# Optimization experiments

Measured on AMD Instinct MI355X. Metric: run time of the kernel, lower is better.

Reference implementation:

```python
import jax, jax.numpy as jnp
import numpy as np
from jax import lax

V, E, H, B, T = 50000, 512, 512, 128, 256
OUT = 2

def gru(x, Wi, Wh, bi, bh):
    # x: [B,T,D]; PyTorch GRU equations, h0 = 0. Returns all hidden states [B,T,H].
    Bsz = x.shape[0]
    Hd = Wh.shape[1]
    xW = jnp.einsum('btd,gd->btg', x, Wi) + bi  # [B,T,3H], precompute input projections
    def step(h, xw):
        gh = h @ Wh.T + bh
        xr, xz, xn = jnp.split(xw, 3, axis=-1)
        hr, hz, hn = jnp.split(gh, 3, axis=-1)
        r = jax.nn.sigmoid(xr + hr)
        z = jax.nn.sigmoid(xz + hz)
        n = jnp.tanh(xn + r * hn)
        h_new = (1.0 - z) * n + z * h
        return h_new, h_new
    h0 = jnp.zeros((Bsz, Hd), x.dtype)
    _, hs = lax.scan(step, h0, jnp.swapaxes(xW, 0, 1))
    return jnp.swapaxes(hs, 0, 1)

def dual_attention(u, r, u_all_sum, Aw, bw, Ww):
    # u, r: [B,T,D] (query side / response side per timestep, vectorized over T).
    # w_t[b,t] = (u A^T + b) . r  (the original bmm of [B,1,D] x [B,D,1])
    w = jnp.einsum('btd,btd->bt', jnp.einsum('btd,ed->bte', u, Aw) + bw, r)
    # score = softmax over D of tanh(w) * Ww  (Linear(1, D, bias=False))
    sc = jax.nn.softmax(jnp.tanh(w)[..., None] * Ww[None, None, :], axis=-1)  # [B,T,D]
    # sum_s embed[b,s,:] * score[b,t,:] = score * (sum over time) ; then * r_t
    return sc * u_all_sum[:, None, :] * r  # [B,T,D]

def setup_inputs() -> dict:
    key = jax.random.key(0)
    ks = jax.random.split(key, 24)
    d = {}
    d['ask'] = jax.random.randint(ks[0], (B, T), 0, V, dtype=jnp.int32)
    d['answer'] = jax.random.randint(ks[1], (B, T), 0, V, dtype=jnp.int32)
    d['ask_keyword'] = jax.random.randint(ks[2], (B, T), 0, V, dtype=jnp.int32)
    d['answer_keyword'] = jax.random.randint(ks[3], (B, T), 0, V, dtype=jnp.int32)
    d['embed'] = jax.random.normal(ks[4], (V, E), jnp.float32) * 0.02
    # GRU 1: input E -> hidden H
    d['Wi1'] = jax.random.normal(ks[5], (3 * H, E), jnp.float32) * 0.05
    d['Wh1'] = jax.random.normal(ks[6], (3 * H, H), jnp.float32) * 0.05
    d['bi1'] = jnp.zeros((3 * H,), jnp.float32)
    d['bh1'] = jnp.zeros((3 * H,), jnp.float32)
    # word attention: Linear(E,E) + Linear(1,E,bias=False)
    d['Aw'] = jax.random.normal(ks[7], (E, E), jnp.float32) * 0.05
    d['bw'] = jnp.zeros((E,), jnp.float32)
    d['Ww'] = jax.random.normal(ks[8], (E,), jnp.float32) * 0.05
    # seq attention: Linear(H,H) + Linear(1,H,bias=False)
    d['As'] = jax.random.normal(ks[9], (H, H), jnp.float32) * 0.05
    d['bs'] = jnp.zeros((H,), jnp.float32)
    d['Ws'] = jax.random.normal(ks[10], (H,), jnp.float32) * 0.05
    # GRU 2: input E+H -> hidden H
    d['Wi2'] = jax.random.normal(ks[11], (3 * H, E + H), jnp.float32) * 0.05
    d['Wh2'] = jax.random.normal(ks[12], (3 * H, H), jnp.float32) * 0.05
    d['bi2'] = jnp.zeros((3 * H,), jnp.float32)
    d['bh2'] = jnp.zeros((3 * H,), jnp.float32)
    # final classifier
    d['Wf'] = jax.random.normal(ks[13], (OUT, H), jnp.float32) * 0.05
    d['bf'] = jnp.zeros((OUT,), jnp.float32)
    return d

def reference(ask, answer, ask_keyword, answer_keyword, embed, Wi1, Wh1, bi1, bh1,
              Aw, bw, Ww, As, bs, Ws, Wi2, Wh2, bi2, bh2, Wf, bf):
    ask_e = embed[ask]            # [B,T,E]
    ans_e = embed[answer]
    ask_kw = embed[ask_keyword]
    ans_kw = embed[answer_keyword]
    h_ask = gru(ask_e, Wi1, Wh1, bi1, bh1)  # [B,T,H]
    h_ans = gru(ans_e, Wi1, Wh1, bi1, bh1)
    # dual attention, vectorized over the original Python loop over t
    ctx_word = dual_attention(ask_kw, ans_kw, ask_kw.sum(axis=1), Aw, bw, Ww)   # [B,T,E]
    ctx_seq = dual_attention(h_ask, h_ans, h_ask.sum(axis=1), As, bs, Ws)       # [B,T,H]
    v = jnp.concatenate([ctx_word, ctx_seq], axis=-1)  # [B,T,E+H]
    h2 = gru(v, Wi2, Wh2, bi2, bh2)[:, -1, :]  # final hidden state [B,H]
    # dropout is identity in eval mode
    return jax.nn.softmax(h2 @ Wf.T + bf, axis=1)
```

## Files before the change

kernel.cpp:

```cpp
#include <hip/hip_runtime.h>
#include <cstdio>

typedef __bf16 bf16x8 __attribute__((ext_vector_type(8)));
typedef float f32x4 __attribute__((ext_vector_type(4)));

#define DEV __device__ __forceinline__

DEV short f2bf(float f) {
    unsigned u = __builtin_bit_cast(unsigned, f);
    u += 0x7fffu + ((u >> 16) & 1u);
    return (short)(u >> 16);
}
DEV float bf2f(short s) {
    unsigned u = ((unsigned)(unsigned short)s) << 16;
    return __builtin_bit_cast(float, u);
}
DEV float sigmoidf_(float x) { return 1.0f / (1.0f + __expf(-x)); }
DEV float tanhf_(float x) { float e = __expf(2.0f * x); return 1.0f - 2.0f / (e + 1.0f); }

DEV void gload_lds16(const void* g, void* l) {
    __builtin_amdgcn_global_load_lds(
        (__attribute__((address_space(1))) void*)(g),
        (__attribute__((address_space(3))) void*)(l), 16, 0, 0);
}
DEV f32x4 mfma16(bf16x8 a, bf16x8 b, f32x4 c) {
    return __builtin_amdgcn_mfma_f32_16x16x32_bf16(a, b, c, 0, 0, 0);
}
DEV unsigned ald(const unsigned* p) {
    return __hip_atomic_load(p, __ATOMIC_RELAXED, __HIP_MEMORY_SCOPE_AGENT);
}
DEV unsigned long long ald64(const void* p) {
    return __hip_atomic_load((const unsigned long long*)p, __ATOMIC_RELAXED, __HIP_MEMORY_SCOPE_AGENT);
}
DEV void ast64(void* p, unsigned long long v) {
    __hip_atomic_store((unsigned long long*)p, v, __ATOMIC_RELAXED, __HIP_MEMORY_SCOPE_AGENT);
}
DEV void ast32(void* p, unsigned v) {
    __hip_atomic_store((unsigned*)p, v, __ATOMIC_RELAXED, __HIP_MEMORY_SCOPE_AGENT);
}
DEV void aadd(unsigned* p, unsigned v) {
    __hip_atomic_fetch_add(p, v, __ATOMIC_RELAXED, __HIP_MEMORY_SCOPE_AGENT);
}

__global__ void f2bf_vec(const float* __restrict__ in, short* __restrict__ out, int n4) {
    int i = blockIdx.x * 256 + threadIdx.x;
    if (i >= n4) return;
    float4 v = reinterpret_cast<const float4*>(in)[i];
    short4 o;
    o.x = f2bf(v.x); o.y = f2bf(v.y); o.z = f2bf(v.z); o.w = f2bf(v.w);
    reinterpret_cast<short4*>(out)[i] = o;
}

__global__ void pack_wh(const float* __restrict__ Wh, short* __restrict__ Wp) {
    int tile = blockIdx.x, kk = blockIdx.y, l = threadIdx.x;
    int n = tile * 16 + (l & 15);
    int k0 = kk * 32 + (l >> 4) * 8;
    const float* src = Wh + (size_t)n * 512 + k0;
    short o[8];
#pragma unroll
    for (int e = 0; e < 8; e++) o[e] = f2bf(src[e]);
    *(int4*)(Wp + ((size_t)(tile * 16 + kk) * 64 + l) * 8) = *(int4*)o;
}

enum { A_XW1 = 0, A_UAW = 1, A_UAS = 2, A_XW2 = 3 };

template<int MODE>
DEV void gemm_tile(short* Als, short* Bls, short* Ct, int m0, int n0,
                   const short* Abase, const short* A2,
                   const int* tok0, const int* tok1,
                   const short* W, const float* bias, short* C, int N, int K)
{
    int tid = threadIdx.x;
    int l = tid & 63, w = tid >> 6;
    int wm = (w >> 1) * 64, wn = (w & 1) * 64;
    int kc = (tid & 7) * 8;

    const short* arow[4];
#pragma unroll
    for (int i = 0; i < 4; i++) {
        int gm = m0 + i * 32 + (tid >> 3);
        if (MODE == A_XW1) {
            int t = gm >> 8, s = gm & 255;
            int tok = (s < 128) ? tok0[s * 256 + t] : tok1[(s - 128) * 256 + t];
            arow[i] = Abase + (size_t)tok * 512;
        } else if (MODE == A_UAW) {
            int t = gm >> 7, b = gm & 127;
            arow[i] = Abase + (size_t)tok0[b * 256 + t] * 512;
        } else if (MODE == A_UAS) {
            int t = gm >> 7, b = gm & 127;
            arow[i] = Abase + ((size_t)t * 256 + b) * 512;
        } else {
            arow[i] = Abase + (size_t)gm * 512;
        }
    }

    f32x4 acc[4][4] = {};
    for (int kt = 0; kt < K; kt += 64) {
#pragma unroll
        for (int i = 0; i < 4; i++) {
            const short* asrc;
            if (MODE == A_XW2) {
                int gm = m0 + i * 32 + (tid >> 3);
                const short* base = (kt < 512) ? Abase : A2;
                asrc = base + (size_t)gm * 512 + (kt & 511) + kc;
            } else {
                asrc = arow[i] + kt + kc;
            }
            gload_lds16(asrc, Als + i * 2048 + tid * 8);
        }
#pragma unroll
        for (int i = 0; i < 4; i++)
            gload_lds16(W + (size_t)(n0 + i * 32 + (tid >> 3)) * K + kt + kc,
                        Bls + i * 2048 + tid * 8);
        __syncthreads();
#pragma unroll
        for (int kk = 0; kk < 2; kk++) {
            int ko = kk * 32 + (l >> 4) * 8;
            bf16x8 af[4], bfr[4];
#pragma unroll
            for (int mi = 0; mi < 4; mi++)
                af[mi] = *(const bf16x8*)&Als[(wm + mi * 16 + (l & 15)) * 64 + ko];
#pragma unroll
            for (int ni = 0; ni < 4; ni++)
                bfr[ni] = *(const bf16x8*)&Bls[(wn + ni * 16 + (l & 15)) * 64 + ko];
#pragma unroll
            for (int mi = 0; mi < 4; mi++)
#pragma unroll
                for (int ni = 0; ni < 4; ni++)
                    acc[mi][ni] = mfma16(af[mi], bfr[ni], acc[mi][ni]);
        }
        __syncthreads();
    }
#pragma unroll
    for (int ni = 0; ni < 4; ni++) {
        float bv = bias[n0 + wn + ni * 16 + (l & 15)];
#pragma unroll
        for (int mi = 0; mi < 4; mi++)
#pragma unroll
            for (int jj = 0; jj < 4; jj++)
                Ct[(wm + mi * 16 + (l >> 4) * 4 + jj) * 132 + wn + ni * 16 + (l & 15)] =
                    f2bf(acc[mi][ni][jj] + bv);
    }
    __syncthreads();
    for (int r = 0; r < 16; r++) {
        int idx = r * 256 + tid;
        int row = idx >> 5, cc = idx & 31;
        unsigned long long val = *(const unsigned long long*)(Ct + row * 132 + cc * 4);
        ast64(C + (size_t)(m0 + row) * N + n0 + cc * 4, val);
    }
    __syncthreads();
}

DEV void embed_sum_dev(const short* ebf, const int* tok, float* out, int b) {
    int d = threadIdx.x;
    float a0 = 0.f, a1 = 0.f;
    for (int t = 0; t < 256; t++) {
        const short* row = ebf + (size_t)tok[b * 256 + t] * 512;
        a0 += bf2f(row[d]); a1 += bf2f(row[d + 256]);
    }
    ast32(&out[b * 512 + d], __builtin_bit_cast(unsigned, a0));
    ast32(&out[b * 512 + d + 256], __builtin_bit_cast(unsigned, a1));
}
DEV void hall_sum_dev(const short* h_all, float* out, int b) {
    int d = threadIdx.x;
    float a0 = 0.f, a1 = 0.f;
    for (int t = 0; t < 256; t++) {
        const short* row = h_all + ((size_t)t * 256 + b) * 512;
        a0 += bf2f(row[d]); a1 += bf2f(row[d + 256]);
    }
    ast32(&out[b * 512 + d], __builtin_bit_cast(unsigned, a0));
    ast32(&out[b * 512 + d + 256], __builtin_bit_cast(unsigned, a1));
}

template<int WORD, int COHOUT>
DEV void combine4(int bb, const short* uA, const short* rsrc, const int* rtok,
                  const float* usum, const float* Wv, short* ctx)
{
    int l = threadIdx.x & 63, w = threadIdx.x >> 6;
    int m = bb * 4 + w;
    int t = m >> 7, b = m & 127;
    const short* rrow;
    if (WORD) rrow = rsrc + (size_t)rtok[b * 256 + t] * 512;
    else      rrow = rsrc + ((size_t)t * 256 + 128 + b) * 512;
    int d0 = l * 8;
    short ru[8], uu[8];
    *(int4*)ru = *(const int4*)(rrow + d0);
    *(unsigned long long*)uu       = ald64(uA + (size_t)m * 512 + d0);
    *((unsigned long long*)uu + 1) = ald64(uA + (size_t)m * 512 + d0 + 4);
    float rv[8], dot = 0.f;
#pragma unroll
    for (int i = 0; i < 8; i++) { rv[i] = bf2f(ru[i]); dot += rv[i] * bf2f(uu[i]); }
#pragma unroll
    for (int off = 32; off >= 1; off >>= 1) dot += __shfl_xor(dot, off);
    float tw = tanhf_(dot);
    float us[8];
#pragma unroll
    for (int i = 0; i < 4; i++) {
        unsigned long long uv = ald64(usum + b * 512 + d0 + i * 2);
        us[i * 2]     = __builtin_bit_cast(float, (unsigned)(uv & 0xffffffffu));
        us[i * 2 + 1] = __builtin_bit_cast(float, (unsigned)(uv >> 32));
    }
    float e[8], se = 0.f;
#pragma unroll
    for (int i = 0; i < 8; i++) { e[i] = __expf(tw * Wv[d0 + i]); se += e[i]; }
#pragma unroll
    for (int off = 32; off >= 1; off >>= 1) se += __shfl_xor(se, off);
    float inv = 1.f / se;
    short ov[8];
#pragma unroll
    for (int i = 0; i < 8; i++) ov[i] = f2bf(e[i] * inv * us[i] * rv[i]);
    if (COHOUT) {
        ast64(ctx + (size_t)m * 512 + d0,     *(unsigned long long*)ov);
        ast64(ctx + (size_t)m * 512 + d0 + 4, *((unsigned long long*)ov + 1));
    } else {
        *(int4*)(ctx + (size_t)m * 512 + d0) = *(int4*)ov;
    }
}

template<int WRITE_ALL>
DEV void scan_role(char* smem, int cb, int rg,
                   const short* xW, const short* Wp, const float* bh,
                   short* hb0, short* hb1, short* h_all, float* h_final,
                   unsigned* done, unsigned* slice_cnt, int tps, int S, int T)
{
    char* wl = smem;
    char* sl = smem + 98304;
    char* ho = smem + 131072;
    int tid = threadIdx.x;
    int r0 = rg * 32;
    int w = tid >> 6, l = tid & 63;
    int rt = w >> 1, ct = w & 1;
    int lrow = l & 15, lq = l >> 4;
    int colg = cb * 32 + ct * 16 + lrow;
    unsigned* mydone = done + rg * 32;

    for (int rr = 0; rr < 24; rr++) {
        int flat = rr * 256 + tid;
        int lane = flat & 63, kk = (flat >> 6) & 15, lg = flat >> 10;
        int g = lg >> 1, c2 = lg & 1;
        gload_lds16(Wp + (((size_t)(g * 32 + cb * 2 + c2) * 16 + kk) * 64 + lane) * 8,
                    wl + flat * 16);
    }
    float bhv[3];
#pragma unroll
    for (int g = 0; g < 3; g++) bhv[g] = bh[g * 512 + colg];
    __syncthreads();

    float hp[4] = {};

    for (int t = 0; t < T; t++) {
        if (tid < 16) {
            if (t > 0)
                while (ald(&mydone[tid]) < (unsigned)t) __builtin_amdgcn_s_sleep(1);
        } else if (tid == 16) {
            while (ald(&slice_cnt[t]) < (unsigned)tps) __builtin_amdgcn_s_sleep(1);
        }
        __syncthreads();

        short xrv[4], xzv[4], xnv[4];
        const short* xbase = xW + ((size_t)t * S + r0) * 1536 + colg;
#pragma unroll
        for (int j = 0; j < 4; j++) {
            const short* xp = xbase + (size_t)(rt * 16 + lq * 4 + j) * 1536;
            xrv[j] = xp[0]; xzv[j] = xp[512]; xnv[j] = xp[1024];
        }

        f32x4 acc[3] = {};
        if (t > 0) {
            const short* hprev = ((t & 1) ? hb0 : hb1) + (size_t)r0 * 512;
            unsigned long long v[16];
            const unsigned long long* sp = (const unsigned long long*)hprev;
#pragma unroll
            for (int k = 0; k < 16; k++)
                v[k] = ald64(sp + k * 256 + tid);
#pragma unroll
            for (int k = 0; k < 16; k++) {
                int off = (k * 256 + tid) * 8;
                int row = off >> 10, colb = off & 1023;
                *(unsigned long long*)(sl + row * 1024 + (colb ^ ((row & 7) << 4))) = v[k];
            }
            __syncthreads();
            bf16x8 afr[16];
            int ar = rt * 16 + lrow;
#pragma unroll
            for (int kk = 0; kk < 16; kk++) {
                int colb = kk * 64 + lq * 16;
                afr[kk] = *(const bf16x8*)(sl + ar * 1024 + (colb ^ ((ar & 7) << 4)));
            }
#pragma unroll
            for (int g = 0; g < 3; g++) {
                const char* bbase = wl + (size_t)((g * 2 + ct) * 16) * 1024 + l * 16;
#pragma unroll
                for (int kk = 0; kk < 16; kk++) {
                    bf16x8 bfr = *(const bf16x8*)(bbase + kk * 1024);
                    acc[g] = mfma16(afr[kk], bfr, acc[g]);
                }
            }
        }

        float hv[4];
#pragma unroll
        for (int j = 0; j < 4; j++) {
            float r = sigmoidf_(bf2f(xrv[j]) + bhv[0] + acc[0][j]);
            float z = sigmoidf_(bf2f(xzv[j]) + bhv[1] + acc[1][j]);
            float n = tanhf_(bf2f(xnv[j]) + r * (acc[2][j] + bhv[2]));
            hv[j] = (1.f - z) * n + z * hp[j];
            hp[j] = hv[j];
            *(short*)(ho + (rt * 16 + lq * 4 + j) * 72 + (ct * 16 + lrow) * 2) = f2bf(hv[j]);
        }
        __syncthreads();
        {
            int row = tid >> 3, ch = tid & 7;
            unsigned long long val = *(const unsigned long long*)(ho + row * 72 + ch * 8);
            short* hnew = (t & 1) ? hb1 : hb0;
            ast64(hnew + (size_t)(r0 + row) * 512 + cb * 32 + ch * 4, val);
            if (WRITE_ALL)
                *(unsigned long long*)(h_all + ((size_t)t * S + r0 + row) * 512 + cb * 32 + ch * 4) = val;
        }
        if (!WRITE_ALL && t == T - 1) {
#pragma unroll
            for (int j = 0; j < 4; j++)
                h_final[(size_t)(r0 + rt * 16 + lq * 4 + j) * 512 + colg] = hv[j];
        }
        __syncthreads();
        if (tid == 0)
            ast32(&mydone[cb], (unsigned)(t + 1));
    }
}

__global__ __launch_bounds__(256, 1) void gru_fused1(
    short* xW1, const short* __restrict__ Wp, const float* __restrict__ bh,
    short* __restrict__ hb0, short* __restrict__ hb1, short* __restrict__ h_all,
    unsigned* done, unsigned* slc,
    const short* __restrict__ embed_bf, const int* __restrict__ ask,
    const int* __restrict__ answer, const short* __restrict__ Wi1b,
    const float* __restrict__ bi1,
    const int* __restrict__ askkw, const int* __restrict__ anskw,
    const short* __restrict__ Awb, const float* __restrict__ bw,
    float* usumW, short* uAb, const float* __restrict__ Ww, short* ctxW,
    unsigned* wcnt)
{
    __shared__ char smem[133376];
    int bid = blockIdx.x, tid = threadIdx.x;

    if (bid >= 128) {
        int pid = bid - 128;
        short* Als = (short*)smem;
        short* Bls = (short*)(smem + 16384);
        short* Ct  = (short*)(smem + 32768);
        for (int q = pid; q < 256 * 24; q += 128) {
            int slice = q / 24, j = q % 24;
            int m0 = (slice * 2 + (j >= 12 ? 1 : 0)) * 128, n0 = (j % 12) * 128;
            gemm_tile<A_XW1>(Als, Bls, Ct, m0, n0, embed_bf, nullptr, ask, answer,
                             Wi1b, bi1, xW1, 1536, 512);
            if (tid == 0) aadd(&slc[slice], 1u);
        }
        embed_sum_dev(embed_bf, askkw, usumW, pid);
        for (int k = 0; k < 8; k++) {
            int q = pid + k * 128;
            gemm_tile<A_UAW>(Als, Bls, Ct, (q >> 2) * 128, (q & 3) * 128,
                             embed_bf, nullptr, askkw, nullptr, Awb, bw, uAb, 512, 512);
        }
        if (tid == 0) {
            aadd(wcnt, 1u);
            while (ald(wcnt) < 128u) __builtin_amdgcn_s_sleep(1);
        }
        __syncthreads();
        for (int bb = pid * 64; bb < pid * 64 + 64; bb++)
            combine4<1, 0>(bb, uAb, embed_bf, anskw, usumW, Ww, ctxW);
        return;
    }
    scan_role<1>(smem, bid & 15, bid >> 4, xW1, Wp, bh, hb0, hb1, h_all, nullptr,
                 done, slc, 24, 256, 256);
}

__global__ __launch_bounds__(256, 1) void gru_fused2(
    short* xW2, const short* __restrict__ Wp, const float* __restrict__ bh,
    short* __restrict__ hb0, short* __restrict__ hb1, float* __restrict__ h_final,
    unsigned* done, unsigned* slc,
    const short* __restrict__ h_all, float* usumS, short* uAb,
    const short* __restrict__ Asb, const float* __restrict__ bs,
    const float* __restrict__ Ws, short* ctxS, const short* __restrict__ ctxW,
    const short* __restrict__ Wi2b, const float* __restrict__ bi2,
    unsigned* acnt, unsigned* ccnt)
{
    __shared__ char smem[133376];
    int bid = blockIdx.x, tid = threadIdx.x;
    short* Als = (short*)smem;
    short* Bls = (short*)(smem + 16384);
    short* Ct  = (short*)(smem + 32768);

    if (bid < 128) hall_sum_dev(h_all, usumS, bid);
    for (int k = 0; k < 4; k++) {
        int q = bid + k * 256;
        gemm_tile<A_UAS>(Als, Bls, Ct, (q >> 2) * 128, (q & 3) * 128,
                         h_all, nullptr, nullptr, nullptr, Asb, bs, uAb, 512, 512);
    }
    if (tid == 0) {
        aadd(acnt, 1u);
        while (ald(acnt) < 256u) __builtin_amdgcn_s_sleep(1);
    }
    __syncthreads();
    for (int bb = bid * 32; bb < bid * 32 + 32; bb++)
        combine4<0, 1>(bb, uAb, h_all, nullptr, usumS, Ws, ctxS);
    __syncthreads();
    if (tid == 0) aadd(ccnt, 1u);

    if (bid >= 64) {
        int pid = bid - 64;
        if (tid == 0) { while (ald(ccnt) < 256u) __builtin_amdgcn_s_sleep(1); }
        __syncthreads();
        for (int q = pid; q < 256 * 12; q += 192) {
            int slice = q / 12, j = q % 12;
            gemm_tile<A_XW2>(Als, Bls, Ct, slice * 128, j * 128,
                             ctxW, ctxS, nullptr, nullptr, Wi2b, bi2, xW2, 1536, 1024);
            if (tid == 0) aadd(&slc[slice], 1u);
        }
        return;
    }
    scan_role<0>(smem, bid & 15, bid >> 4, xW2, Wp, bh, hb0, hb1, nullptr, h_final,
                 done, slc, 12, 128, 256);
}

__global__ void final_head_k(const float* __restrict__ h2, const float* __restrict__ Wf,
                             const float* __restrict__ bfv, float* __restrict__ out) {
    int b = blockIdx.x, l = threadIdx.x;
    float d0 = 0.f, d1 = 0.f;
    for (int k = l; k < 512; k += 64) {
        float h = h2[b * 512 + k];
        d0 += h * Wf[k];
        d1 += h * Wf[512 + k];
    }
#pragma unroll
    for (int off = 32; off >= 1; off >>= 1) { d0 += __shfl_xor(d0, off); d1 += __shfl_xor(d1, off); }
    if (l == 0) {
        float l0 = d0 + bfv[0], l1 = d1 + bfv[1];
        float mx = fmaxf(l0, l1);
        float e0 = __expf(l0 - mx), e1 = __expf(l1 - mx);
        float s = e0 + e1;
        out[b * 2] = e0 / s; out[b * 2 + 1] = e1 / s;
    }
}

extern "C" void kernel_launch(void* const* d_in, const int* in_sizes, int n_in,
                              void* d_out, int out_size, void* d_ws, size_t ws_size,
                              hipStream_t stream)
{
    const int* ask    = (const int*)d_in[0];
    const int* answer = (const int*)d_in[1];
    const int* askkw  = (const int*)d_in[2];
    const int* anskw  = (const int*)d_in[3];
    const float* embed = (const float*)d_in[4];
    const float* Wi1 = (const float*)d_in[5];
    const float* Wh1 = (const float*)d_in[6];
    const float* bi1 = (const float*)d_in[7];
    const float* bh1 = (const float*)d_in[8];
    const float* Aw  = (const float*)d_in[9];
    const float* bw  = (const float*)d_in[10];
    const float* Ww  = (const float*)d_in[11];
    const float* As  = (const float*)d_in[12];
    const float* bs  = (const float*)d_in[13];
    const float* Ws  = (const float*)d_in[14];
    const float* Wi2 = (const float*)d_in[15];
    const float* Wh2 = (const float*)d_in[16];
    const float* bi2 = (const float*)d_in[17];
    const float* bh2 = (const float*)d_in[18];
    const float* Wf  = (const float*)d_in[19];
    const float* bfv = (const float*)d_in[20];

    char* ws = (char*)d_ws;
    size_t off = 0;
    auto alloc = [&](size_t bytes) -> void* {
        void* p = (void*)(ws + off);
        off += (bytes + 255) & ~(size_t)255;
        return p;
    };
    short* embed_bf = (short*)alloc(50000ULL * 512 * 2);
    short* Wi1b = (short*)alloc(1536 * 512 * 2);
    short* Wp1  = (short*)alloc(1536 * 512 * 2);
    short* Awb  = (short*)alloc(512 * 512 * 2);
    short* Asb  = (short*)alloc(512 * 512 * 2);
    short* Wi2b = (short*)alloc(1536 * 1024 * 2);
    short* Wp2  = (short*)alloc(1536 * 512 * 2);
    char* X = (char*)alloc(201326592ULL);
    short* xW1  = (short*)X;
    short* xW2  = (short*)X;
    short* ctxS = (short*)(X + 100663296);
    short* uAb  = (short*)alloc(32768ULL * 512 * 2);
    short* ctxW = (short*)alloc(32768ULL * 512 * 2);
    short* h_all = (short*)alloc(256ULL * 256 * 512 * 2);
    short* hb0 = (short*)alloc(256 * 512 * 2);
    short* hb1 = (short*)alloc(256 * 512 * 2);
    float* usumW = (float*)alloc(128 * 512 * 4);
    float* usumS = (float*)alloc(128 * 512 * 4);
    float* h2f   = (float*)alloc(128 * 512 * 4);
    unsigned* syncb = (unsigned*)alloc((8 * 32 + 4 * 32 + 256 + 256 + 96) * 4);
    unsigned* done1 = syncb;
    unsigned* done2 = syncb + 8 * 32;
    unsigned* slc1  = syncb + 12 * 32;
    unsigned* slc2  = slc1 + 256;
    unsigned* wcnt1 = slc2 + 256;
    unsigned* acnt2 = wcnt1 + 32;
    unsigned* ccnt2 = wcnt1 + 64;

    if (off > ws_size) {
        fprintf(stderr, "kernel_launch: workspace too small: need %zu have %zu\n", off, ws_size);
        return;
    }

    hipMemsetAsync(syncb, 0, (8 * 32 + 4 * 32 + 256 + 256 + 96) * 4, stream);

    auto cv = [&](const float* src, short* dst, int n) {
        int n4 = n / 4;
        f2bf_vec<<<(n4 + 255) / 256, 256, 0, stream>>>(src, dst, n4);
    };
    cv(embed, embed_bf, 50000 * 512);
    cv(Wi1, Wi1b, 1536 * 512);
    cv(Aw, Awb, 512 * 512);
    cv(As, Asb, 512 * 512);
    cv(Wi2, Wi2b, 1536 * 1024);
    pack_wh<<<dim3(96, 16), 64, 0, stream>>>(Wh1, Wp1);
    pack_wh<<<dim3(96, 16), 64, 0, stream>>>(Wh2, Wp2);

    {
        void* args[] = { (void*)&xW1, (void*)&Wp1, (void*)&bh1, (void*)&hb0, (void*)&hb1,
                         (void*)&h_all, (void*)&done1, (void*)&slc1,
                         (void*)&embed_bf, (void*)&ask, (void*)&answer, (void*)&Wi1b, (void*)&bi1,
                         (void*)&askkw, (void*)&anskw, (void*)&Awb, (void*)&bw,
                         (void*)&usumW, (void*)&uAb, (void*)&Ww, (void*)&ctxW, (void*)&wcnt1 };
        hipError_t e = hipLaunchCooperativeKernel(
            reinterpret_cast<void*>(&gru_fused1), dim3(256), dim3(256), args, 0, stream);
        if (e != hipSuccess)
            gru_fused1<<<256, 256, 0, stream>>>(
                xW1, Wp1, bh1, hb0, hb1, h_all, done1, slc1,
                embed_bf, ask, answer, Wi1b, bi1,
                askkw, anskw, Awb, bw, usumW, uAb, Ww, ctxW, wcnt1);
    }

    {
        void* args[] = { (void*)&xW2, (void*)&Wp2, (void*)&bh2, (void*)&hb0, (void*)&hb1,
                         (void*)&h2f, (void*)&done2, (void*)&slc2,
                         (void*)&h_all, (void*)&usumS, (void*)&uAb,
                         (void*)&Asb, (void*)&bs, (void*)&Ws, (void*)&ctxS, (void*)&ctxW,
                         (void*)&Wi2b, (void*)&bi2, (void*)&acnt2, (void*)&ccnt2 };
        hipError_t e = hipLaunchCooperativeKernel(
            reinterpret_cast<void*>(&gru_fused2), dim3(256), dim3(256), args, 0, stream);
        if (e != hipSuccess)
            gru_fused2<<<256, 256, 0, stream>>>(
                xW2, Wp2, bh2, hb0, hb1, h2f, done2, slc2,
                h_all, usumS, uAb, Asb, bs, Ws, ctxS, ctxW, Wi2b, bi2, acnt2, ccnt2);
    }

    final_head_k<<<128, 64, 0, stream>>>(h2f, Wf, bfv, (float*)d_out);
}
```

Baseline: 1.930 ms.

## Replace per-step done counters with timestep-tagged hidden-state words in GRU scan

Each bf16 hidden value is now stored in a 32-bit word together with a 16-bit timestep tag. Consumers spin on the data itself until the tags match, instead of waiting on per-block done counters. This drops the LDS staging of the output tile, two __syncthreads, and the separate flag store and poll per step, so each step's handoff costs one round trip. In exchange the hidden-state exchange traffic doubles, stores become scattered 32-bit writes, the tag buffers must be zeroed, and GRU2 uses a tag base offset so it does not mistake GRU1's leftover tags for its own.

```diff
diff --git a/kernel.cpp b/kernel.cpp
--- a/kernel.cpp
+++ b/kernel.cpp
@@ -220,19 +220,19 @@
 template<int WRITE_ALL>
 DEV void scan_role(char* smem, int cb, int rg,
                    const short* xW, const short* Wp, const float* bh,
-                   short* hb0, short* hb1, short* h_all, float* h_final,
-                   unsigned* done, unsigned* slice_cnt, int tps, int S, int T)
+                   unsigned* hbt0, unsigned* hbt1,
+                   short* h_all, float* h_final,
+                   unsigned* slice_cnt, int tps, int S, int T, int tagbase)
 {
     char* wl = smem;
     char* sl = smem + 98304;
-    char* ho = smem + 131072;
     int tid = threadIdx.x;
     int r0 = rg * 32;
     int w = tid >> 6, l = tid & 63;
     int rt = w >> 1, ct = w & 1;
     int lrow = l & 15, lq = l >> 4;
     int colg = cb * 32 + ct * 16 + lrow;
-    unsigned* mydone = done + rg * 32;
+    const unsigned long long TMASK = 0xFFFF0000FFFF0000ULL;
 
     for (int rr = 0; rr < 24; rr++) {
         int flat = rr * 256 + tid;
@@ -249,10 +249,26 @@
     float hp[4] = {};
 
     for (int t = 0; t < T; t++) {
-        if (tid < 16) {
-            if (t > 0)
-                while (ald(&mydone[tid]) < (unsigned)t) __builtin_amdgcn_s_sleep(1);
-        } else if (tid == 16) {
+        if (t > 0) {
+            const unsigned* hbp = ((t & 1) ? hbt0 : hbt1) + (size_t)r0 * 512;
+            const unsigned long long* sp = (const unsigned long long*)hbp;
+            unsigned long long tg = (unsigned long long)(unsigned)(tagbase + t);
+            unsigned long long pat = (tg << 16) | (tg << 48);
+            unsigned long long v[32];
+#pragma unroll
+            for (int k = 0; k < 32; k++) v[k] = ald64(sp + k * 256 + tid);
+#pragma unroll
+            for (int k = 0; k < 32; k++) {
+                while (((v[k] ^ pat) & TMASK) != 0ULL) {
+                    __builtin_amdgcn_s_sleep(1);
+                    v[k] = ald64(sp + k * 256 + tid);
+                }
+                unsigned lo = (unsigned)v[k] & 0xFFFFu;
+                unsigned hi = (unsigned)(v[k] >> 32) & 0xFFFFu;
+                *(unsigned*)(sl + k * 1024 + ((tid * 4) ^ ((k & 7) << 4))) = lo | (hi << 16);
+            }
+        }
+        if (tid == 0) {
             while (ald(&slice_cnt[t]) < (unsigned)tps) __builtin_amdgcn_s_sleep(1);
         }
         __syncthreads();
@@ -267,19 +283,6 @@
 
         f32x4 acc[3] = {};
         if (t > 0) {
-            const short* hprev = ((t & 1) ? hb0 : hb1) + (size_t)r0 * 512;
-            unsigned long long v[16];
-            const unsigned long long* sp = (const unsigned long long*)hprev;
-#pragma unroll
-            for (int k = 0; k < 16; k++)
-                v[k] = ald64(sp + k * 256 + tid);
-#pragma unroll
-            for (int k = 0; k < 16; k++) {
-                int off = (k * 256 + tid) * 8;
-                int row = off >> 10, colb = off & 1023;
-                *(unsigned long long*)(sl + row * 1024 + (colb ^ ((row & 7) << 4))) = v[k];
-            }
-            __syncthreads();
             bf16x8 afr[16];
             int ar = rt * 16 + lrow;
 #pragma unroll
@@ -298,6 +301,8 @@
             }
         }
 
+        unsigned* hbn = ((t & 1) ? hbt1 : hbt0);
+        unsigned tagw = (unsigned)(tagbase + t + 1) << 16;
         float hv[4];
 #pragma unroll
         for (int j = 0; j < 4; j++) {
@@ -306,32 +311,20 @@
             float n = tanhf_(bf2f(xnv[j]) + r * (acc[2][j] + bhv[2]));
             hv[j] = (1.f - z) * n + z * hp[j];
             hp[j] = hv[j];
-            *(short*)(ho + (rt * 16 + lq * 4 + j) * 72 + (ct * 16 + lrow) * 2) = f2bf(hv[j]);
+            short hb16 = f2bf(hv[j]);
+            int row = r0 + rt * 16 + lq * 4 + j;
+            ast32(hbn + (size_t)row * 512 + colg, tagw | (unsigned)(unsigned short)hb16);
+            if (WRITE_ALL) h_all[((size_t)t * S + row) * 512 + colg] = hb16;
+            else if (t == T - 1) h_final[(size_t)row * 512 + colg] = hv[j];
         }
         __syncthreads();
-        {
-            int row = tid >> 3, ch = tid & 7;
-            unsigned long long val = *(const unsigned long long*)(ho + row * 72 + ch * 8);
-            short* hnew = (t & 1) ? hb1 : hb0;
-            ast64(hnew + (size_t)(r0 + row) * 512 + cb * 32 + ch * 4, val);
-            if (WRITE_ALL)
-                *(unsigned long long*)(h_all + ((size_t)t * S + r0 + row) * 512 + cb * 32 + ch * 4) = val;
-        }
-        if (!WRITE_ALL && t == T - 1) {
-#pragma unroll
-            for (int j = 0; j < 4; j++)
-                h_final[(size_t)(r0 + rt * 16 + lq * 4 + j) * 512 + colg] = hv[j];
-        }
-        __syncthreads();
-        if (tid == 0)
-            ast32(&mydone[cb], (unsigned)(t + 1));
     }
 }
 
 __global__ __launch_bounds__(256, 1) void gru_fused1(
     short* xW1, const short* __restrict__ Wp, const float* __restrict__ bh,
-    short* __restrict__ hb0, short* __restrict__ hb1, short* __restrict__ h_all,
-    unsigned* done, unsigned* slc,
+    unsigned* hbt0, unsigned* hbt1, short* __restrict__ h_all,
+    unsigned* slc,
     const short* __restrict__ embed_bf, const int* __restrict__ ask,
     const int* __restrict__ answer, const short* __restrict__ Wi1b,
     const float* __restrict__ bi1,
@@ -340,7 +333,7 @@
     float* usumW, short* uAb, const float* __restrict__ Ww, short* ctxW,
     unsigned* wcnt)
 {
-    __shared__ char smem[133376];
+    __shared__ char smem[131072];
     int bid = blockIdx.x, tid = threadIdx.x;
 
     if (bid >= 128) {
@@ -370,21 +363,21 @@
             combine4<1, 0>(bb, uAb, embed_bf, anskw, usumW, Ww, ctxW);
         return;
     }
-    scan_role<1>(smem, bid & 15, bid >> 4, xW1, Wp, bh, hb0, hb1, h_all, nullptr,
-                 done, slc, 24, 256, 256);
+    scan_role<1>(smem, bid & 15, bid >> 4, xW1, Wp, bh, hbt0, hbt1, h_all, nullptr,
+                 slc, 24, 256, 256, 0);
 }
 
 __global__ __launch_bounds__(256, 1) void gru_fused2(
     short* xW2, const short* __restrict__ Wp, const float* __restrict__ bh,
-    short* __restrict__ hb0, short* __restrict__ hb1, float* __restrict__ h_final,
-    unsigned* done, unsigned* slc,
+    unsigned* hbt0, unsigned* hbt1, float* __restrict__ h_final,
+    unsigned* slc,
     const short* __restrict__ h_all, float* usumS, short* uAb,
     const short* __restrict__ Asb, const float* __restrict__ bs,
     const float* __restrict__ Ws, short* ctxS, const short* __restrict__ ctxW,
     const short* __restrict__ Wi2b, const float* __restrict__ bi2,
     unsigned* acnt, unsigned* ccnt)
 {
-    __shared__ char smem[133376];
+    __shared__ char smem[131072];
     int bid = blockIdx.x, tid = threadIdx.x;
     short* Als = (short*)smem;
     short* Bls = (short*)(smem + 16384);
@@ -418,8 +411,8 @@
         }
         return;
     }
-    scan_role<0>(smem, bid & 15, bid >> 4, xW2, Wp, bh, hb0, hb1, nullptr, h_final,
-                 done, slc, 12, 128, 256);
+    scan_role<0>(smem, bid & 15, bid >> 4, xW2, Wp, bh, hbt0, hbt1, nullptr, h_final,
+                 slc, 12, 128, 256, 256);
 }
 
 __global__ void final_head_k(const float* __restrict__ h2, const float* __restrict__ Wf,
@@ -489,17 +482,15 @@
     short* uAb  = (short*)alloc(32768ULL * 512 * 2);
     short* ctxW = (short*)alloc(32768ULL * 512 * 2);
     short* h_all = (short*)alloc(256ULL * 256 * 512 * 2);
-    short* hb0 = (short*)alloc(256 * 512 * 2);
-    short* hb1 = (short*)alloc(256 * 512 * 2);
+    unsigned* hbt0 = (unsigned*)alloc(256 * 512 * 4);
+    unsigned* hbt1 = (unsigned*)alloc(256 * 512 * 4);
     float* usumW = (float*)alloc(128 * 512 * 4);
     float* usumS = (float*)alloc(128 * 512 * 4);
     float* h2f   = (float*)alloc(128 * 512 * 4);
-    unsigned* syncb = (unsigned*)alloc((8 * 32 + 4 * 32 + 256 + 256 + 96) * 4);
-    unsigned* done1 = syncb;
-    unsigned* done2 = syncb + 8 * 32;
-    unsigned* slc1  = syncb + 12 * 32;
-    unsigned* slc2  = slc1 + 256;
-    unsigned* wcnt1 = slc2 + 256;
+    unsigned* syncb = (unsigned*)alloc((256 + 256 + 96) * 4);
+    unsigned* slc1  = syncb;
+    unsigned* slc2  = syncb + 256;
+    unsigned* wcnt1 = syncb + 512;
     unsigned* acnt2 = wcnt1 + 32;
     unsigned* ccnt2 = wcnt1 + 64;
 
@@ -508,7 +499,9 @@
         return;
     }
 
-    hipMemsetAsync(syncb, 0, (8 * 32 + 4 * 32 + 256 + 256 + 96) * 4, stream);
+    hipMemsetAsync(syncb, 0, (256 + 256 + 96) * 4, stream);
+    hipMemsetAsync(hbt0, 0, 256 * 512 * 4, stream);
+    hipMemsetAsync(hbt1, 0, 256 * 512 * 4, stream);
 
     auto cv = [&](const float* src, short* dst, int n) {
         int n4 = n / 4;
@@ -523,8 +516,8 @@
     pack_wh<<<dim3(96, 16), 64, 0, stream>>>(Wh2, Wp2);
 
     {
-        void* args[] = { (void*)&xW1, (void*)&Wp1, (void*)&bh1, (void*)&hb0, (void*)&hb1,
-                         (void*)&h_all, (void*)&done1, (void*)&slc1,
+        void* args[] = { (void*)&xW1, (void*)&Wp1, (void*)&bh1, (void*)&hbt0, (void*)&hbt1,
+                         (void*)&h_all, (void*)&slc1,
                          (void*)&embed_bf, (void*)&ask, (void*)&answer, (void*)&Wi1b, (void*)&bi1,
                          (void*)&askkw, (void*)&anskw, (void*)&Awb, (void*)&bw,
                          (void*)&usumW, (void*)&uAb, (void*)&Ww, (void*)&ctxW, (void*)&wcnt1 };
@@ -532,14 +525,14 @@
             reinterpret_cast<void*>(&gru_fused1), dim3(256), dim3(256), args, 0, stream);
         if (e != hipSuccess)
             gru_fused1<<<256, 256, 0, stream>>>(
-                xW1, Wp1, bh1, hb0, hb1, h_all, done1, slc1,
+                xW1, Wp1, bh1, hbt0, hbt1, h_all, slc1,
                 embed_bf, ask, answer, Wi1b, bi1,
                 askkw, anskw, Awb, bw, usumW, uAb, Ww, ctxW, wcnt1);
     }
 
     {
-        void* args[] = { (void*)&xW2, (void*)&Wp2, (void*)&bh2, (void*)&hb0, (void*)&hb1,
-                         (void*)&h2f, (void*)&done2, (void*)&slc2,
+        void* args[] = { (void*)&xW2, (void*)&Wp2, (void*)&bh2, (void*)&hbt0, (void*)&hbt1,
+                         (void*)&h2f, (void*)&slc2,
                          (void*)&h_all, (void*)&usumS, (void*)&uAb,
                          (void*)&Asb, (void*)&bs, (void*)&Ws, (void*)&ctxS, (void*)&ctxW,
                          (void*)&Wi2b, (void*)&bi2, (void*)&acnt2, (void*)&ccnt2 };
@@ -547,7 +540,7 @@
             reinterpret_cast<void*>(&gru_fused2), dim3(256), dim3(256), args, 0, stream);
         if (e != hipSuccess)
             gru_fused2<<<256, 256, 0, stream>>>(
-                xW2, Wp2, bh2, hb0, hb1, h2f, done2, slc2,
+                xW2, Wp2, bh2, hbt0, hbt1, h2f, slc2,
                 h_all, usumS, uAb, Asb, bs, Ws, ctxS, ctxW, Wi2b, bi2, acnt2, ccnt2);
     }
 
```

After: 6.120 ms. 3.17x slower.
